# Kernel optimization log

Hardware: AMD Instinct MI355X
Metric: run time of the kernel (lower is better)

Reference implementation:

```python
import jax, jax.numpy as jnp
import numpy as np


def setup_inputs() -> dict:
    key = jax.random.key(0)
    ks = jax.random.split(key, 5)
    B, N, C, H = 8, 8192, 512, 8
    scale = 1.0 / np.sqrt(C)
    return {
        "x": jax.random.normal(ks[0], (B, N, C), dtype=jnp.float32),
        "qk_w": jax.random.normal(ks[1], (2 * C, C), dtype=jnp.float32) * scale,
        "qk_b": jax.random.normal(ks[2], (2 * C,), dtype=jnp.float32) * 0.01,
        "lepe_w": jax.random.normal(ks[3], (C, 1, 3), dtype=jnp.float32) * 0.5,
        "lepe_b": jax.random.normal(ks[4], (C,), dtype=jnp.float32) * 0.01,
        "num_heads": H,
    }


def reference(x, qk_w, qk_b, lepe_w, lepe_b, num_heads):
    B, N, C = x.shape
    hd = C // num_heads
    # qk projection -> split into q, k; ELU(.)+1 feature map
    qk = x @ qk_w.T + qk_b                      # [B,N,2C]
    q = jax.nn.elu(qk[..., :C]) + 1.0
    k = jax.nn.elu(qk[..., C:]) + 1.0
    q = q.reshape(B, N, num_heads, hd).transpose(0, 2, 1, 3)  # [B,H,N,hd]
    k = k.reshape(B, N, num_heads, hd).transpose(0, 2, 1, 3)
    v = x.reshape(B, N, num_heads, hd).transpose(0, 2, 1, 3)
    # normalizer: z = 1 / (q . mean_n(k) + eps)
    k_mean = k.mean(axis=2)                                    # [B,H,hd]
    z = 1.0 / (jnp.einsum('bhnd,bhd->bhn', q, k_mean) + 1e-6)  # [B,H,N]
    # linear attention: kv = k^T v per head, then q @ kv
    kv = jnp.einsum('bhnd,bhne->bhde', k, v)                   # [B,H,hd,hd]
    attn = jnp.einsum('bhnd,bhde->bhne', q, kv) * z[..., None] # [B,H,N,hd]
    attn = attn.transpose(0, 2, 1, 3).reshape(B, N, C)
    # lepe: depthwise conv1d over tokens on v (== x after head reshape round-trip)
    vc = x.transpose(0, 2, 1)                                  # [B,C,N]
    lepe = jax.lax.conv_general_dilated(
        vc, lepe_w, window_strides=(1,), padding=((1, 1),),
        dimension_numbers=('NCH', 'OIH', 'NCH'), feature_group_count=C,
    ) + lepe_b[None, :, None]                                  # [B,C,N]
    return attn + lepe.transpose(0, 2, 1)
```

## Files before the change

kernel.cpp:

```cpp
#include <hip/hip_runtime.h>
#include <hip/hip_bf16.h>

#define B_    8
#define N_    8192
#define C_    512
#define H_    8
#define HD_   64
#define M_    (B_ * N_)
#define TWO_C 1024

typedef short short8 __attribute__((ext_vector_type(8)));
typedef float f32x4  __attribute__((ext_vector_type(4)));

__device__ __forceinline__ float bf2f(unsigned v) {
    return __uint_as_float(v << 16);
}

__device__ __forceinline__ unsigned f2bf(float f) {
    union { __hip_bfloat16 b; unsigned short u; } cv;
    cv.b = __float2bfloat16(f);
    return (unsigned)cv.u;
}

__device__ __forceinline__ uint2 pack4(float4 f) {
    uint2 r;
    r.x = f2bf(f.x) | (f2bf(f.y) << 16);
    r.y = f2bf(f.z) | (f2bf(f.w) << 16);
    return r;
}

__device__ __forceinline__ short8 pack8(float4 lo, float4 hi) {
    uint2 a = pack4(lo), b = pack4(hi);
    union { uint4 u; short8 s; } cv;
    cv.u = make_uint4(a.x, a.y, b.x, b.y);
    return cv.s;
}

__global__ __launch_bounds__(256) void conv_w_bf16(
    const float* __restrict__ w, unsigned short* __restrict__ wbf)
{
    const int i = (blockIdx.x * 256 + threadIdx.x) * 8;
    float4 a = *(const float4*)(w + i);
    float4 b = *(const float4*)(w + i + 4);
    uint2 pa = pack4(a), pb = pack4(b);
    *(uint4*)(wbf + i) = make_uint4(pa.x, pa.y, pb.x, pb.y);
}

__global__ __launch_bounds__(256) void conv_x_bf16(
    const float* __restrict__ x, unsigned short* __restrict__ xbf)
{
    const size_t i = ((size_t)blockIdx.x * 256 + threadIdx.x) * 8;
    float4 a = *(const float4*)(x + i);
    float4 b = *(const float4*)(x + i + 4);
    uint2 pa = pack4(a), pb = pack4(b);
    *(uint4*)(xbf + i) = make_uint4(pa.x, pa.y, pb.x, pb.y);
}

__global__ __launch_bounds__(256, 2) void gemm_qk_mfma(
    const unsigned short* __restrict__ xbf, const unsigned short* __restrict__ wbf,
    const float* __restrict__ bias,
    __hip_bfloat16* __restrict__ qws, __hip_bfloat16* __restrict__ kws)
{
    __shared__ __align__(16) unsigned short As[128 * 64];
    __shared__ __align__(16) unsigned short Bs[128 * 64];

    const int t  = threadIdx.x;
    const int wv = t >> 6;
    const int ln = t & 63;

    const int L  = blockIdx.x;
    const int rp = (L & 7) + ((L >> 6) << 3);
    const int cp = (L >> 3) & 7;
    const int m0 = rp * 128;
    const int n0 = cp * 128;

    const int wm = wv & 1, wn = wv >> 1;
    const int fr = ln & 15;
    const int qg = ln >> 4;

    const int sr = t >> 3;
    const int ss = t & 7;
    const int ds = ss ^ (sr & 7);

    f32x4 acc[4][4];
#pragma unroll
    for (int i = 0; i < 4; i++)
#pragma unroll
        for (int j = 0; j < 4; j++) acc[i][j] = {0.f, 0.f, 0.f, 0.f};

    const unsigned short* xa = xbf + (size_t)(m0 + sr) * C_ + ss * 8;
    const unsigned short* wa = wbf + (size_t)(n0 + sr) * C_ + ss * 8;
    unsigned short* const la = &As[sr * 64 + ds * 8];
    unsigned short* const lb = &Bs[sr * 64 + ds * 8];

    for (int k0 = 0; k0 < C_; k0 += 64) {
        uint4 a0 = *(const uint4*)(xa + k0);
        uint4 a1 = *(const uint4*)(xa + k0 + (size_t)32 * C_);
        uint4 a2 = *(const uint4*)(xa + k0 + (size_t)64 * C_);
        uint4 a3 = *(const uint4*)(xa + k0 + (size_t)96 * C_);
        uint4 b0 = *(const uint4*)(wa + k0);
        uint4 b1 = *(const uint4*)(wa + k0 + (size_t)32 * C_);
        uint4 b2 = *(const uint4*)(wa + k0 + (size_t)64 * C_);
        uint4 b3 = *(const uint4*)(wa + k0 + (size_t)96 * C_);
        if (k0) __syncthreads();
        *(uint4*)(la + 0 * 32 * 64) = a0;
        *(uint4*)(la + 1 * 32 * 64) = a1;
        *(uint4*)(la + 2 * 32 * 64) = a2;
        *(uint4*)(la + 3 * 32 * 64) = a3;
        *(uint4*)(lb + 0 * 32 * 64) = b0;
        *(uint4*)(lb + 1 * 32 * 64) = b1;
        *(uint4*)(lb + 2 * 32 * 64) = b2;
        *(uint4*)(lb + 3 * 32 * 64) = b3;
        __syncthreads();

        short8 af[4][2], bfr[4][2];
#pragma unroll
        for (int i = 0; i < 4; i++) {
            const int r = wm * 64 + i * 16 + fr;
#pragma unroll
            for (int kk = 0; kk < 2; kk++) {
                const int slot = (kk * 4 + qg) ^ (fr & 7);
                af[i][kk] = *(const short8*)&As[r * 64 + slot * 8];
            }
        }
#pragma unroll
        for (int j = 0; j < 4; j++) {
            const int r = wn * 64 + j * 16 + fr;
#pragma unroll
            for (int kk = 0; kk < 2; kk++) {
                const int slot = (kk * 4 + qg) ^ (fr & 7);
                bfr[j][kk] = *(const short8*)&Bs[r * 64 + slot * 8];
            }
        }
#pragma unroll
        for (int i = 0; i < 4; i++)
#pragma unroll
            for (int j = 0; j < 4; j++)
#pragma unroll
                for (int kk = 0; kk < 2; kk++)
                    acc[i][j] = __builtin_amdgcn_mfma_f32_16x16x32_bf16(
                        af[i][kk], bfr[j][kk], acc[i][j], 0, 0, 0);
    }

    __hip_bfloat16* dst;
    int oc0;
    if (n0 < C_) { dst = qws; oc0 = n0; }
    else         { dst = kws; oc0 = n0 - C_; }
    float bv[4];
#pragma unroll
    for (int j = 0; j < 4; j++) bv[j] = bias[n0 + wn * 64 + j * 16 + fr];
    const int rb = (ln >> 4) * 4;
#pragma unroll
    for (int i = 0; i < 4; i++) {
#pragma unroll
        for (int r = 0; r < 4; r++) {
            const size_t m = (size_t)(m0 + wm * 64 + i * 16 + rb + r);
#pragma unroll
            for (int j = 0; j < 4; j++) {
                const int oc = oc0 + wn * 64 + j * 16 + fr;
                float v = acc[i][j][r] + bv[j];
                v = (v > 0.f) ? (v + 1.f) : __expf(v);
                dst[m * C_ + oc] = __float2bfloat16(v);
            }
        }
    }
}

__global__ __launch_bounds__(256) void kv_partial(
    const __hip_bfloat16* __restrict__ kws, const float* __restrict__ x,
    float* __restrict__ kvT, float* __restrict__ kmean)
{
    __shared__ float kt[32][64];
    __shared__ float vt[32][64];
    const int t  = threadIdx.x;
    const int s  = blockIdx.x;
    const int bh = blockIdx.y;
    const int b  = bh >> 3, h = bh & 7;
    const int td = t >> 4, te = t & 15;
    const int kr = t >> 3;
    const int kc = (t & 7) * 8;
    const int vr = t >> 4;
    const int vc = (t & 15) * 4;

    const size_t base = (size_t)b * N_ * C_ + h * HD_;

    float acc[4][4];
    float ksum[4] = {0.f, 0.f, 0.f, 0.f};
#pragma unroll
    for (int i = 0; i < 4; i++)
#pragma unroll
        for (int j = 0; j < 4; j++) acc[i][j] = 0.f;

    const int nstart = s * (N_ / 16);
    for (int n0 = nstart; n0 < nstart + N_ / 16; n0 += 32) {
        uint4  ku = *(const uint4*)&kws[base + (size_t)(n0 + kr) * C_ + kc];
        float4 v0 = *(const float4*)&x[base + (size_t)(n0 + vr) * C_ + vc];
        float4 v1 = *(const float4*)&x[base + (size_t)(n0 + vr + 16) * C_ + vc];
        __syncthreads();
        kt[kr][kc + 0] = bf2f(ku.x & 0xffffu); kt[kr][kc + 1] = bf2f(ku.x >> 16);
        kt[kr][kc + 2] = bf2f(ku.y & 0xffffu); kt[kr][kc + 3] = bf2f(ku.y >> 16);
        kt[kr][kc + 4] = bf2f(ku.z & 0xffffu); kt[kr][kc + 5] = bf2f(ku.z >> 16);
        kt[kr][kc + 6] = bf2f(ku.w & 0xffffu); kt[kr][kc + 7] = bf2f(ku.w >> 16);
        *(float4*)&vt[vr][vc]      = v0;
        *(float4*)&vt[vr + 16][vc] = v1;
        __syncthreads();
#pragma unroll
        for (int nn = 0; nn < 32; nn++) {
            float4 kd = *(const float4*)&kt[nn][td * 4];
            float4 ve = *(const float4*)&vt[nn][te * 4];
            float kr4[4] = {kd.x, kd.y, kd.z, kd.w};
            float vr4[4] = {ve.x, ve.y, ve.z, ve.w};
#pragma unroll
            for (int i = 0; i < 4; i++)
#pragma unroll
                for (int j = 0; j < 4; j++) acc[i][j] += kr4[i] * vr4[j];
            ksum[0] += kd.x; ksum[1] += kd.y; ksum[2] += kd.z; ksum[3] += kd.w;
        }
    }

    float* kvp = kvT + (size_t)bh * HD_ * HD_;
#pragma unroll
    for (int i = 0; i < 4; i++)
#pragma unroll
        for (int j = 0; j < 4; j++)
            atomicAdd(&kvp[(te * 4 + j) * HD_ + td * 4 + i], acc[i][j]);
    if (te == 0) {
#pragma unroll
        for (int i = 0; i < 4; i++)
            atomicAdd(&kmean[bh * HD_ + td * 4 + i], ksum[i] * (1.0f / N_));
    }
}

__global__ __launch_bounds__(256, 4) void out_mfma(
    const __hip_bfloat16* __restrict__ qws, const float* __restrict__ x,
    const float* __restrict__ kvT, const float* __restrict__ kmean,
    const float* __restrict__ lw, const float* __restrict__ lb,
    float* __restrict__ out)
{
    __shared__ __align__(16) unsigned short qs[128][72];
    __shared__ __align__(16) unsigned short xsb[130][68];
    __shared__ float lw0[64], lw1[64], lw2[64], lbs[64];

    const int t  = threadIdx.x;
    const int n0 = blockIdx.x * 128;
    const int bh = blockIdx.y;
    const int b  = bh >> 3, h = bh & 7;

    const int wv = t >> 6, ln = t & 63;
    const int fr = ln & 15;
    const int fk = (ln >> 4) * 8;

    {
        const __hip_bfloat16* qp = qws + ((size_t)b * N_ + n0) * C_ + h * HD_;
        for (int i = t; i < 1024; i += 256) {
            const int r = i >> 3, c8 = (i & 7) * 8;
            uint4 u = *(const uint4*)&qp[(size_t)r * C_ + c8];
            *(uint4*)&qs[r][c8] = u;
        }
    }
    {
        for (int i = t; i < 130 * 16; i += 256) {
            const int r = i >> 4, c4 = (i & 15) * 4;
            const int n = n0 - 1 + r;
            float4 v = make_float4(0.f, 0.f, 0.f, 0.f);
            if (n >= 0 && n < N_)
                v = *(const float4*)&x[((size_t)b * N_ + n) * C_ + h * HD_ + c4];
            *(uint2*)&xsb[r][c4] = pack4(v);
        }
    }
    if (t < 64) {
        const int c = h * HD_ + t;
        lw0[t] = lw[c * 3 + 0];
        lw1[t] = lw[c * 3 + 1];
        lw2[t] = lw[c * 3 + 2];
        lbs[t] = lb[c];
    }

    short8 bfr[4][2], bz[2];
    {
        const float* kvp = kvT + (size_t)bh * 4096;
#pragma unroll
        for (int c = 0; c < 4; c++)
#pragma unroll
            for (int kk = 0; kk < 2; kk++) {
                const float* p = kvp + (c * 16 + fr) * 64 + kk * 32 + fk;
                float4 lo = *(const float4*)p;
                float4 hi = *(const float4*)(p + 4);
                bfr[c][kk] = pack8(lo, hi);
            }
        const float* kmp = kmean + bh * HD_;
        const short8 z8 = {0, 0, 0, 0, 0, 0, 0, 0};
#pragma unroll
        for (int kk = 0; kk < 2; kk++) {
            const float* p = kmp + kk * 32 + fk;
            float4 lo = *(const float4*)p;
            float4 hi = *(const float4*)(p + 4);
            short8 pk = pack8(lo, hi);
            bz[kk] = (fr == 0) ? pk : z8;
        }
    }

    __syncthreads();

    const int r0 = wv * 32;

    f32x4 acc[2][4], zacc[2];
#pragma unroll
    for (int bd = 0; bd < 2; bd++) {
        zacc[bd] = {0.f, 0.f, 0.f, 0.f};
#pragma unroll
        for (int c = 0; c < 4; c++) acc[bd][c] = {0.f, 0.f, 0.f, 0.f};
    }

    short8 af[2][2];
#pragma unroll
    for (int bd = 0; bd < 2; bd++)
#pragma unroll
        for (int kk = 0; kk < 2; kk++)
            af[bd][kk] = *(const short8*)&qs[r0 + bd * 16 + fr][kk * 32 + fk];

#pragma unroll
    for (int bd = 0; bd < 2; bd++) {
#pragma unroll
        for (int c = 0; c < 4; c++)
#pragma unroll
            for (int kk = 0; kk < 2; kk++)
                acc[bd][c] = __builtin_amdgcn_mfma_f32_16x16x32_bf16(
                    af[bd][kk], bfr[c][kk], acc[bd][c], 0, 0, 0);
#pragma unroll
        for (int kk = 0; kk < 2; kk++)
            zacc[bd] = __builtin_amdgcn_mfma_f32_16x16x32_bf16(
                af[bd][kk], bz[kk], zacc[bd], 0, 0, 0);
    }

    const int rb = (ln >> 4) * 4;
#pragma unroll
    for (int bd = 0; bd < 2; bd++) {
        float zr[4];
#pragma unroll
        for (int r = 0; r < 4; r++)
            zr[r] = 1.0f / (__shfl(zacc[bd][r], ln & 48) + 1e-6f);
#pragma unroll
        for (int c = 0; c < 4; c++) {
            const int e = c * 16 + fr;
            const float w0 = lw0[e], w1 = lw1[e], w2 = lw2[e], bb = lbs[e];
#pragma unroll
            for (int r = 0; r < 4; r++) {
                const int nn = r0 + bd * 16 + rb + r;
                const float le = bf2f(xsb[nn][e]) * w0 + bf2f(xsb[nn + 1][e]) * w1
                               + bf2f(xsb[nn + 2][e]) * w2 + bb;
                out[((size_t)b * N_ + n0 + nn) * C_ + h * HD_ + e] =
                    acc[bd][c][r] * zr[r] + le;
            }
        }
    }
}

extern "C" void kernel_launch(void* const* d_in, const int* in_sizes, int n_in,
                              void* d_out, int out_size, void* d_ws, size_t ws_size,
                              hipStream_t stream)
{
    const float* x      = (const float*)d_in[0];
    const float* qk_w   = (const float*)d_in[1];
    const float* qk_b   = (const float*)d_in[2];
    const float* lepe_w = (const float*)d_in[3];
    const float* lepe_b = (const float*)d_in[4];
    float* out = (float*)d_out;

    char* ws = (char*)d_ws;
    __hip_bfloat16* qws = (__hip_bfloat16*)ws;
    __hip_bfloat16* kws = qws + (size_t)M_ * C_;
    float* kvT   = (float*)(ws + 2 * (size_t)M_ * C_ * sizeof(__hip_bfloat16));
    float* kmean = kvT + (size_t)64 * HD_ * HD_;
    unsigned short* wbf = (unsigned short*)kvT;
    unsigned short* xbf = (unsigned short*)d_out;

    conv_w_bf16<<<256, 256, 0, stream>>>(qk_w, wbf);
    conv_x_bf16<<<M_ * C_ / (256 * 8), 256, 0, stream>>>(x, xbf);
    gemm_qk_mfma<<<4096, 256, 0, stream>>>(xbf, wbf, qk_b, qws, kws);
    hipMemsetAsync(kvT, 0, (size_t)(64 * HD_ * HD_ + 64 * HD_) * sizeof(float),
                   stream);
    kv_partial<<<dim3(16, 64), 256, 0, stream>>>(kws, x, kvT, kmean);
    out_mfma<<<dim3(N_ / 128, B_ * H_), 256, 0, stream>>>(
        qws, x, kvT, kmean, lepe_w, lepe_b, out);
}
```

Baseline: 497.5 us.

## Compute per-head K^T V partials with bf16 MFMA and read bf16 x

The kv_partial kernel now computes the per-head K^T V partial sums with bf16 MFMA instructions instead of scalar fp32 FMAs. K and V tiles are stored transposed in LDS. The column sums of K for the mean are produced by an extra MFMA against a ones vector. V is read from the bf16 copy of x already sitting in the output buffer, which halves the V read traffic but lowers V precision to bf16 in the kv accumulation. One pass is ~8 % of run time, so the total effect is bounded.

```diff
diff --git a/kernel.cpp b/kernel.cpp
--- a/kernel.cpp
+++ b/kernel.cpp
@@ -166,68 +166,112 @@
     }
 }
 
-__global__ __launch_bounds__(256) void kv_partial(
-    const __hip_bfloat16* __restrict__ kws, const float* __restrict__ x,
+__global__ __launch_bounds__(256, 4) void kv_partial(
+    const __hip_bfloat16* __restrict__ kws, const unsigned short* __restrict__ xbf,
     float* __restrict__ kvT, float* __restrict__ kmean)
 {
-    __shared__ float kt[32][64];
-    __shared__ float vt[32][64];
+    __shared__ __align__(16) unsigned short ktT[64][72];
+    __shared__ __align__(16) unsigned short vtT[64][72];
+
     const int t  = threadIdx.x;
     const int s  = blockIdx.x;
     const int bh = blockIdx.y;
     const int b  = bh >> 3, h = bh & 7;
-    const int td = t >> 4, te = t & 15;
-    const int kr = t >> 3;
-    const int kc = (t & 7) * 8;
-    const int vr = t >> 4;
-    const int vc = (t & 15) * 4;
-
-    const size_t base = (size_t)b * N_ * C_ + h * HD_;
-
-    float acc[4][4];
-    float ksum[4] = {0.f, 0.f, 0.f, 0.f};
-#pragma unroll
-    for (int i = 0; i < 4; i++)
-#pragma unroll
-        for (int j = 0; j < 4; j++) acc[i][j] = 0.f;
+    const int wv = t >> 6, ln = t & 63;
+    const int wm = wv & 1, wn = wv >> 1;
+    const int fr = ln & 15, qg = ln >> 4;
+    const int sd = wv * 16;
+
+    const unsigned short* kp0 = (const unsigned short*)kws + h * HD_ + sd;
+    const unsigned short* vp0 = xbf + h * HD_ + sd;
+
+    f32x4 acc[2][2], zacc[2];
+#pragma unroll
+    for (int i = 0; i < 2; i++) {
+        zacc[i] = {0.f, 0.f, 0.f, 0.f};
+#pragma unroll
+        for (int j = 0; j < 2; j++) acc[i][j] = {0.f, 0.f, 0.f, 0.f};
+    }
+
+    short8 ones;
+    {
+        const unsigned short o = (fr == 0) ? 0x3F80 : 0;
+#pragma unroll
+        for (int j = 0; j < 8; j++) ones[j] = (short)o;
+    }
 
     const int nstart = s * (N_ / 16);
-    for (int n0 = nstart; n0 < nstart + N_ / 16; n0 += 32) {
-        uint4  ku = *(const uint4*)&kws[base + (size_t)(n0 + kr) * C_ + kc];
-        float4 v0 = *(const float4*)&x[base + (size_t)(n0 + vr) * C_ + vc];
-        float4 v1 = *(const float4*)&x[base + (size_t)(n0 + vr + 16) * C_ + vc];
+    for (int tt = 0; tt < 8; tt++) {
+        const size_t row = (size_t)b * N_ + nstart + tt * 64 + ln;
+        uint4 ku0 = *(const uint4*)(kp0 + row * C_);
+        uint4 ku1 = *(const uint4*)(kp0 + row * C_ + 8);
+        uint4 vu0 = *(const uint4*)(vp0 + row * C_);
+        uint4 vu1 = *(const uint4*)(vp0 + row * C_ + 8);
+        if (tt) __syncthreads();
+        {
+            unsigned short* kc = &ktT[sd][ln];
+            unsigned short* vc = &vtT[sd][ln];
+            kc[0 * 72]  = (unsigned short)ku0.x; kc[1 * 72]  = (unsigned short)(ku0.x >> 16);
+            kc[2 * 72]  = (unsigned short)ku0.y; kc[3 * 72]  = (unsigned short)(ku0.y >> 16);
+            kc[4 * 72]  = (unsigned short)ku0.z; kc[5 * 72]  = (unsigned short)(ku0.z >> 16);
+            kc[6 * 72]  = (unsigned short)ku0.w; kc[7 * 72]  = (unsigned short)(ku0.w >> 16);
+            kc[8 * 72]  = (unsigned short)ku1.x; kc[9 * 72]  = (unsigned short)(ku1.x >> 16);
+            kc[10 * 72] = (unsigned short)ku1.y; kc[11 * 72] = (unsigned short)(ku1.y >> 16);
+            kc[12 * 72] = (unsigned short)ku1.z; kc[13 * 72] = (unsigned short)(ku1.z >> 16);
+            kc[14 * 72] = (unsigned short)ku1.w; kc[15 * 72] = (unsigned short)(ku1.w >> 16);
+            vc[0 * 72]  = (unsigned short)vu0.x; vc[1 * 72]  = (unsigned short)(vu0.x >> 16);
+            vc[2 * 72]  = (unsigned short)vu0.y; vc[3 * 72]  = (unsigned short)(vu0.y >> 16);
+            vc[4 * 72]  = (unsigned short)vu0.z; vc[5 * 72]  = (unsigned short)(vu0.z >> 16);
+            vc[6 * 72]  = (unsigned short)vu0.w; vc[7 * 72]  = (unsigned short)(vu0.w >> 16);
+            vc[8 * 72]  = (unsigned short)vu1.x; vc[9 * 72]  = (unsigned short)(vu1.x >> 16);
+            vc[10 * 72] = (unsigned short)vu1.y; vc[11 * 72] = (unsigned short)(vu1.y >> 16);
+            vc[12 * 72] = (unsigned short)vu1.z; vc[13 * 72] = (unsigned short)(vu1.z >> 16);
+            vc[14 * 72] = (unsigned short)vu1.w; vc[15 * 72] = (unsigned short)(vu1.w >> 16);
+        }
         __syncthreads();
-        kt[kr][kc + 0] = bf2f(ku.x & 0xffffu); kt[kr][kc + 1] = bf2f(ku.x >> 16);
-        kt[kr][kc + 2] = bf2f(ku.y & 0xffffu); kt[kr][kc + 3] = bf2f(ku.y >> 16);
-        kt[kr][kc + 4] = bf2f(ku.z & 0xffffu); kt[kr][kc + 5] = bf2f(ku.z >> 16);
-        kt[kr][kc + 6] = bf2f(ku.w & 0xffffu); kt[kr][kc + 7] = bf2f(ku.w >> 16);
-        *(float4*)&vt[vr][vc]      = v0;
-        *(float4*)&vt[vr + 16][vc] = v1;
-        __syncthreads();
-#pragma unroll
-        for (int nn = 0; nn < 32; nn++) {
-            float4 kd = *(const float4*)&kt[nn][td * 4];
-            float4 ve = *(const float4*)&vt[nn][te * 4];
-            float kr4[4] = {kd.x, kd.y, kd.z, kd.w};
-            float vr4[4] = {ve.x, ve.y, ve.z, ve.w};
-#pragma unroll
-            for (int i = 0; i < 4; i++)
-#pragma unroll
-                for (int j = 0; j < 4; j++) acc[i][j] += kr4[i] * vr4[j];
-            ksum[0] += kd.x; ksum[1] += kd.y; ksum[2] += kd.z; ksum[3] += kd.w;
+
+        short8 av[2][2], bk[2][2];
+#pragma unroll
+        for (int i = 0; i < 2; i++)
+#pragma unroll
+            for (int kk = 0; kk < 2; kk++) {
+                av[i][kk] = *(const short8*)&vtT[wm * 32 + i * 16 + fr][kk * 32 + qg * 8];
+                bk[i][kk] = *(const short8*)&ktT[wn * 32 + i * 16 + fr][kk * 32 + qg * 8];
+            }
+#pragma unroll
+        for (int i = 0; i < 2; i++)
+#pragma unroll
+            for (int j = 0; j < 2; j++)
+#pragma unroll
+                for (int kk = 0; kk < 2; kk++)
+                    acc[i][j] = __builtin_amdgcn_mfma_f32_16x16x32_bf16(
+                        av[i][kk], bk[j][kk], acc[i][j], 0, 0, 0);
+        if (wm == 0) {
+#pragma unroll
+            for (int j = 0; j < 2; j++)
+#pragma unroll
+                for (int kk = 0; kk < 2; kk++)
+                    zacc[j] = __builtin_amdgcn_mfma_f32_16x16x32_bf16(
+                        ones, bk[j][kk], zacc[j], 0, 0, 0);
         }
     }
 
     float* kvp = kvT + (size_t)bh * HD_ * HD_;
 #pragma unroll
-    for (int i = 0; i < 4; i++)
-#pragma unroll
-        for (int j = 0; j < 4; j++)
-            atomicAdd(&kvp[(te * 4 + j) * HD_ + td * 4 + i], acc[i][j]);
-    if (te == 0) {
-#pragma unroll
-        for (int i = 0; i < 4; i++)
-            atomicAdd(&kmean[bh * HD_ + td * 4 + i], ksum[i] * (1.0f / N_));
+    for (int i = 0; i < 2; i++)
+#pragma unroll
+        for (int j = 0; j < 2; j++)
+#pragma unroll
+            for (int r = 0; r < 4; r++) {
+                const int e = wm * 32 + i * 16 + qg * 4 + r;
+                const int d = wn * 32 + j * 16 + fr;
+                atomicAdd(&kvp[e * HD_ + d], acc[i][j][r]);
+            }
+    if (wm == 0 && ln < 16) {
+#pragma unroll
+        for (int j = 0; j < 2; j++)
+            atomicAdd(&kmean[bh * HD_ + wn * 32 + j * 16 + fr],
+                      zacc[j][0] * (1.0f / N_));
     }
 }
 
@@ -380,7 +424,7 @@
     gemm_qk_mfma<<<4096, 256, 0, stream>>>(xbf, wbf, qk_b, qws, kws);
     hipMemsetAsync(kvT, 0, (size_t)(64 * HD_ * HD_ + 64 * HD_) * sizeof(float),
                    stream);
-    kv_partial<<<dim3(16, 64), 256, 0, stream>>>(kws, x, kvT, kmean);
+    kv_partial<<<dim3(16, 64), 256, 0, stream>>>(kws, xbf, kvT, kmean);
     out_mfma<<<dim3(N_ / 128, B_ * H_), 256, 0, stream>>>(
         qws, x, kvT, kmean, lepe_w, lepe_b, out);
 }
```

New measurement: 423.8 us. -14.8%, faster.
